# Kernel optimization log

Hardware: AMD Instinct MI355X
Metric: run time of the kernel (lower is better)

## Reference

```python
import jax, jax.numpy as jnp
import numpy as np

OUT, IN = 4096, 4096
N_CODES, SUBD = 4096, 8
N_SUB = IN // SUBD  # 512
N_SPARSE = 65536


def setup_inputs() -> dict:
    key = jax.random.key(0)
    ks = jax.random.split(key, 8)
    inp = {
        "input": jax.random.normal(ks[0], (4, 2048, IN), dtype=jnp.float32),
        "codebooks": jax.random.normal(ks[1], (N_CODES, SUBD), dtype=jnp.float32),
        "mappings": jax.random.randint(ks[2], (OUT, N_SUB), 0, N_CODES, dtype=jnp.int32),
        # identity permutation of columns (a valid subvector assignment)
        "subvector_assignment": jnp.arange(IN, dtype=jnp.int32),
        "rowise_norms": jax.random.uniform(ks[3], (IN,), dtype=jnp.float32) + 0.5,
        "colwise_norms": jax.random.uniform(ks[4], (OUT,), dtype=jnp.float32) + 0.5,
        # unique, sorted flat indices into the OUT*IN weight (stride keeps them unique)
        "sparse_idx": (jnp.arange(N_SPARSE, dtype=jnp.int32) * (OUT * IN // N_SPARSE)).astype(jnp.int32),
        "sparse_parameters": jax.random.normal(ks[5], (N_SPARSE,), dtype=jnp.float32),
        "bias": jax.random.normal(ks[6], (OUT,), dtype=jnp.float32),
    }
    return inp


def _construct_weight(codebooks, mappings, subvector_assignment,
                      rowise_norms, colwise_norms, sparse_idx, sparse_parameters):
    out_f, n_sub = mappings.shape
    in_f = subvector_assignment.shape[0]
    # gather-dequant: [out, n_sub, d] -> [out, in]
    recon = codebooks[mappings].reshape(out_f, n_sub * codebooks.shape[-1])
    w = jnp.zeros((out_f, in_f), dtype=codebooks.dtype).at[:, subvector_assignment].set(recon)
    # note: source names are swapped; rowise broadcasts over rows (len in_f)
    w = rowise_norms[None, :] * colwise_norms[:, None] * w
    # sparse outlier scatter (torch: weight[mask] = sparse_parameters, row-major order)
    w = w.reshape(-1).at[sparse_idx].set(sparse_parameters).reshape(out_f, in_f)
    return w


def reference(input, codebooks, mappings, subvector_assignment,
              rowise_norms, colwise_norms, sparse_idx, sparse_parameters, bias):
    w = _construct_weight(codebooks, mappings, subvector_assignment,
                          rowise_norms, colwise_norms, sparse_idx, sparse_parameters)
    # F.linear: x @ W^T + b
    return jnp.einsum("bsi,oi->bso", input, w) + bias
```

## Files before the change

### kernel.cpp

```cpp
#include <hip/hip_runtime.h>
#include <hip/hip_bf16.h>

#define OUT_F 4096
#define IN_F  4096
#define N_SUB 512
#define SUBD  8
#define M_DIM 8192
#define N_SPARSE 65536

typedef __bf16 bf16x8 __attribute__((ext_vector_type(8)));
typedef float floatx4 __attribute__((ext_vector_type(4)));

__global__ __launch_bounds__(256) void build_weight(
    const float* __restrict__ cb,
    const int*   __restrict__ map,
    const int*   __restrict__ sa,
    const float* __restrict__ rn,
    const float* __restrict__ cn,
    __hip_bfloat16* __restrict__ W)
{
    int t  = blockIdx.x * blockDim.x + threadIdx.x;
    int o  = t >> 9;
    int j8 = t & (N_SUB - 1);
    int code = map[o * N_SUB + j8];
    float cno = cn[o];
    const float* cbp = cb + code * SUBD;
#pragma unroll
    for (int e = 0; e < SUBD; e++) {
        int j = j8 * SUBD + e;
        int i = sa[j];
        float v = cbp[e] * rn[i] * cno;
        W[(long)o * IN_F + i] = __float2bfloat16(v);
    }
}

__global__ __launch_bounds__(256) void sparse_scatter(
    const int*   __restrict__ idx,
    const float* __restrict__ sp,
    __hip_bfloat16* __restrict__ W, int n)
{
    int t = blockIdx.x * blockDim.x + threadIdx.x;
    if (t < n) W[idx[t]] = __float2bfloat16(sp[t]);
}

__global__ __launch_bounds__(256) void cvt_bf16(
    const float* __restrict__ in, __hip_bfloat16* __restrict__ out, long n)
{
    long i = ((long)blockIdx.x * blockDim.x + threadIdx.x) * 8;
    if (i >= n) return;
    float4 f0 = *(const float4*)(in + i);
    float4 f1 = *(const float4*)(in + i + 4);
    union { __hip_bfloat16 h[8]; uint4 u; } pk;
    pk.h[0] = __float2bfloat16(f0.x); pk.h[1] = __float2bfloat16(f0.y);
    pk.h[2] = __float2bfloat16(f0.z); pk.h[3] = __float2bfloat16(f0.w);
    pk.h[4] = __float2bfloat16(f1.x); pk.h[5] = __float2bfloat16(f1.y);
    pk.h[6] = __float2bfloat16(f1.z); pk.h[7] = __float2bfloat16(f1.w);
    *(uint4*)(out + i) = pk.u;
}

__device__ __forceinline__ void gl2lds16(const __hip_bfloat16* g, __hip_bfloat16* l)
{
    __builtin_amdgcn_global_load_lds(
        (const __attribute__((address_space(1))) unsigned int*)g,
        (__attribute__((address_space(3))) unsigned int*)l,
        16, 0, 0);
}

__global__ __launch_bounds__(256) void gemm_bt_bias(
    const __hip_bfloat16* __restrict__ A,
    const __hip_bfloat16* __restrict__ B,
    const float* __restrict__ bias,
    float* __restrict__ C)
{
    constexpr int M = M_DIM, N = OUT_F, K = IN_F;
    constexpr int BK = 32;

    __shared__ __hip_bfloat16 sA[128 * BK];
    __shared__ __hip_bfloat16 sB[128 * BK];

    const int tid  = threadIdx.x;
    const int bm   = blockIdx.y;
    const int bn   = blockIdx.x;
    const int wave = tid >> 6;
    const int lane = tid & 63;
    const int wm   = (wave >> 1) * 64;
    const int wn   = (wave & 1) * 64;
    const int l16  = lane & 15;
    const int quad = lane >> 4;

    floatx4 acc[4][4] = {};

    const int r0 = tid >> 2;
    const int c0 = (tid & 3) * 8;
    const __hip_bfloat16* gA0 = A + (long)(bm * 128 + r0) * K + c0;
    const __hip_bfloat16* gA1 = A + (long)(bm * 128 + 64 + r0) * K + c0;
    const __hip_bfloat16* gB0 = B + (long)(bn * 128 + r0) * K + c0;
    const __hip_bfloat16* gB1 = B + (long)(bn * 128 + 64 + r0) * K + c0;
    __hip_bfloat16* lA0 = sA + tid * 8;
    __hip_bfloat16* lA1 = sA + (tid + 256) * 8;
    __hip_bfloat16* lB0 = sB + tid * 8;
    __hip_bfloat16* lB1 = sB + (tid + 256) * 8;

    for (int kt = 0; kt < K; kt += BK) {
        gl2lds16(gA0 + kt, lA0);
        gl2lds16(gA1 + kt, lA1);
        gl2lds16(gB0 + kt, lB0);
        gl2lds16(gB1 + kt, lB1);
        __syncthreads();

        bf16x8 af[4], bfr[4];
#pragma unroll
        for (int mt = 0; mt < 4; mt++)
            af[mt] = *(const bf16x8*)(sA + (wm + mt * 16 + l16) * BK + quad * 8);
#pragma unroll
        for (int nt = 0; nt < 4; nt++)
            bfr[nt] = *(const bf16x8*)(sB + (wn + nt * 16 + l16) * BK + quad * 8);

#pragma unroll
        for (int mt = 0; mt < 4; mt++)
#pragma unroll
            for (int nt = 0; nt < 4; nt++)
                acc[mt][nt] = __builtin_amdgcn_mfma_f32_16x16x32_bf16(
                    af[mt], bfr[nt], acc[mt][nt], 0, 0, 0);

        __syncthreads();
    }

#pragma unroll
    for (int mt = 0; mt < 4; mt++) {
#pragma unroll
        for (int nt = 0; nt < 4; nt++) {
            int row = bm * 128 + wm + mt * 16 + quad * 4;
            int col = bn * 128 + wn + nt * 16 + l16;
            float bv = bias[col];
            float* cp = C + (long)row * N + col;
#pragma unroll
            for (int r = 0; r < 4; r++)
                cp[(long)r * N] = acc[mt][nt][r] + bv;
        }
    }
}

extern "C" void kernel_launch(void* const* d_in, const int* in_sizes, int n_in,
                              void* d_out, int out_size, void* d_ws, size_t ws_size,
                              hipStream_t stream)
{
    const float* input = (const float*)d_in[0];
    const float* cb    = (const float*)d_in[1];
    const int*   map   = (const int*)  d_in[2];
    const int*   sa    = (const int*)  d_in[3];
    const float* rn    = (const float*)d_in[4];
    const float* cn    = (const float*)d_in[5];
    const int*   sidx  = (const int*)  d_in[6];
    const float* sp    = (const float*)d_in[7];
    const float* bias  = (const float*)d_in[8];
    float* out = (float*)d_out;

    __hip_bfloat16* W  = (__hip_bfloat16*)d_ws;
    __hip_bfloat16* Ab = (__hip_bfloat16*)((char*)d_ws + (size_t)OUT_F * IN_F * 2);

    build_weight<<<(OUT_F * N_SUB) / 256, 256, 0, stream>>>(cb, map, sa, rn, cn, W);
    sparse_scatter<<<N_SPARSE / 256, 256, 0, stream>>>(sidx, sp, W, N_SPARSE);
    const long n_act = (long)M_DIM * IN_F;
    cvt_bf16<<<(int)(n_act / 8 / 256), 256, 0, stream>>>(input, Ab, n_act);
    dim3 grid(OUT_F / 128, M_DIM / 128);
    gemm_bt_bias<<<grid, 256, 0, stream>>>(Ab, W, bias, out);
}
```

Before: 591.3 us.

## Swizzle LDS tile layout in GEMM and vectorize weight build for contiguous assignment

The GEMM now XOR-swizzles which 16-byte chunk of each row is loaded into LDS, and the fragment reads apply the same swizzle. The goal is to cut LDS bank conflicts on the ds_read_b128 fragment loads. The weight builder also checks whether the subvector assignment is contiguous for each 8-element group. When it is, it uses vector loads and a single 16-byte store instead of eight scattered bf16 stores. The swizzle has to match exactly between the global-to-LDS copy and the fragment reads, or results will be wrong.

```diff
diff --git a/kernel.cpp b/kernel.cpp
--- a/kernel.cpp
+++ b/kernel.cpp
@@ -22,15 +22,35 @@
     int t  = blockIdx.x * blockDim.x + threadIdx.x;
     int o  = t >> 9;
     int j8 = t & (N_SUB - 1);
+    int j  = j8 * SUBD;
     int code = map[o * N_SUB + j8];
     float cno = cn[o];
-    const float* cbp = cb + code * SUBD;
+    float4 c0 = *(const float4*)(cb + code * SUBD);
+    float4 c1 = *(const float4*)(cb + code * SUBD + 4);
+    int4 s0 = *(const int4*)(sa + j);
+    int4 s1 = *(const int4*)(sa + j + 4);
+    bool contig = (s0.x == j)     & (s0.y == j + 1) & (s0.z == j + 2) &
+                  (s0.w == j + 3) & (s1.x == j + 4) & (s1.y == j + 5) &
+                  (s1.z == j + 6) & (s1.w == j + 7);
+    if (contig) {
+        float4 r0 = *(const float4*)(rn + j);
+        float4 r1 = *(const float4*)(rn + j + 4);
+        union { __hip_bfloat16 h[8]; uint4 u; } pk;
+        pk.h[0] = __float2bfloat16(c0.x * r0.x * cno);
+        pk.h[1] = __float2bfloat16(c0.y * r0.y * cno);
+        pk.h[2] = __float2bfloat16(c0.z * r0.z * cno);
+        pk.h[3] = __float2bfloat16(c0.w * r0.w * cno);
+        pk.h[4] = __float2bfloat16(c1.x * r1.x * cno);
+        pk.h[5] = __float2bfloat16(c1.y * r1.y * cno);
+        pk.h[6] = __float2bfloat16(c1.z * r1.z * cno);
+        pk.h[7] = __float2bfloat16(c1.w * r1.w * cno);
+        *(uint4*)(W + (long)o * IN_F + j) = pk.u;
+    } else {
+        float c[8] = {c0.x, c0.y, c0.z, c0.w, c1.x, c1.y, c1.z, c1.w};
+        int   s[8] = {s0.x, s0.y, s0.z, s0.w, s1.x, s1.y, s1.z, s1.w};
 #pragma unroll
-    for (int e = 0; e < SUBD; e++) {
-        int j = j8 * SUBD + e;
-        int i = sa[j];
-        float v = cbp[e] * rn[i] * cno;
-        W[(long)o * IN_F + i] = __float2bfloat16(v);
+        for (int e = 0; e < SUBD; e++)
+            W[(long)o * IN_F + s[e]] = __float2bfloat16(c[e] * rn[s[e]] * cno);
     }
 }
 
@@ -72,7 +92,7 @@
     const float* __restrict__ bias,
     float* __restrict__ C)
 {
-    constexpr int M = M_DIM, N = OUT_F, K = IN_F;
+    constexpr int N = OUT_F, K = IN_F;
     constexpr int BK = 32;
 
     __shared__ __hip_bfloat16 sA[128 * BK];
@@ -87,11 +107,12 @@
     const int wn   = (wave & 1) * 64;
     const int l16  = lane & 15;
     const int quad = lane >> 4;
+    const int sw   = l16 & 3;
 
     floatx4 acc[4][4] = {};
 
     const int r0 = tid >> 2;
-    const int c0 = (tid & 3) * 8;
+    const int c0 = (((tid & 3) ^ (r0 & 3)) ) * 8;
     const __hip_bfloat16* gA0 = A + (long)(bm * 128 + r0) * K + c0;
     const __hip_bfloat16* gA1 = A + (long)(bm * 128 + 64 + r0) * K + c0;
     const __hip_bfloat16* gB0 = B + (long)(bn * 128 + r0) * K + c0;
@@ -110,11 +131,15 @@
 
         bf16x8 af[4], bfr[4];
 #pragma unroll
-        for (int mt = 0; mt < 4; mt++)
-            af[mt] = *(const bf16x8*)(sA + (wm + mt * 16 + l16) * BK + quad * 8);
+        for (int mt = 0; mt < 4; mt++) {
+            int row = wm + mt * 16 + l16;
+            af[mt] = *(const bf16x8*)(sA + (row * 4 + (quad ^ sw)) * 8);
+        }
 #pragma unroll
-        for (int nt = 0; nt < 4; nt++)
-            bfr[nt] = *(const bf16x8*)(sB + (wn + nt * 16 + l16) * BK + quad * 8);
+        for (int nt = 0; nt < 4; nt++) {
+            int row = wn + nt * 16 + l16;
+            bfr[nt] = *(const bf16x8*)(sB + (row * 4 + (quad ^ sw)) * 8);
+        }
 
 #pragma unroll
         for (int mt = 0; mt < 4; mt++)
```

After: 560.6 us. 1.05x faster.
